# Optimization experiments

Measured on AMD Instinct MI355X. Metric: run time of the kernel, lower is better.

Reference implementation:

```python
import jax, jax.numpy as jnp
import numpy as np

D_IN = 1024
D_H = 1024
B = 8
T = 4096


def setup_inputs() -> dict:
    key = jax.random.key(0)
    ks = jax.random.split(key, 7)
    s_in = 1.0 / np.sqrt(D_IN)
    s_h = 1.0 / np.sqrt(D_H)
    return {
        "x": jax.random.normal(ks[0], (B, T, D_IN), dtype=jnp.float32),
        "h0": jnp.zeros((B, D_H), dtype=jnp.float32),
        "W_a": jax.random.normal(ks[1], (D_IN, D_H), dtype=jnp.float32) * s_in,
        "b_a": jax.random.normal(ks[2], (D_H,), dtype=jnp.float32),
        "W_b": jax.random.normal(ks[3], (D_IN, D_H), dtype=jnp.float32) * s_in,
        "W_y": jax.random.normal(ks[4], (D_H, D_H), dtype=jnp.float32) * s_h,
        "W_skip": jax.random.normal(ks[5], (D_IN, D_H), dtype=jnp.float32) * s_in,
    }


def reference(x, h0, W_a, b_a, W_b, W_y, W_skip):
    # forward_map f: X -> H (monoid element = (decay a, accumulated input b))
    a = jax.nn.sigmoid(jnp.einsum("btd,de->bte", x, W_a) + b_a)  # [B,T,D_H]
    b = jnp.einsum("btd,de->bte", x, W_b)                        # [B,T,D_H]

    # prepend initial carry as monoid element (1, h0), then associative scan
    a_all = jnp.concatenate([jnp.ones_like(h0)[:, None, :], a], axis=1)  # [B,T+1,D_H]
    b_all = jnp.concatenate([h0[:, None, :], b], axis=1)                 # [B,T+1,D_H]

    def monoid_op(l, r):
        a1, b1 = l
        a2, b2 = r
        return (a1 * a2, a2 * b1 + b2)

    _, h_all = jax.lax.associative_scan(monoid_op, (a_all, b_all), axis=1)
    next_h = h_all[:, 1:]  # [B,T,D_H] recurrent states

    # backward_map g: H x X -> Y
    y = jnp.einsum("btd,de->bte", jax.nn.gelu(next_h), W_y) + jnp.einsum("btd,de->bte", x, W_skip)
    return (next_h, y)
```

## Files before the change

### kernel.cpp

```cpp
#include <hip/hip_runtime.h>
#include <stdint.h>

#define D_HID 1024
#define BATCH 8
#define TLEN 4096
#define M_ROWS (BATCH*TLEN)
#define CHUNK 128
#define NCHUNK (TLEN/CHUNK)

typedef __attribute__((ext_vector_type(8))) short s8v;
typedef __attribute__((ext_vector_type(4))) float f4v;

__device__ __forceinline__ ushort f2bf(float x){
  uint32_t u = __builtin_bit_cast(uint32_t, x);
  uint32_t r = u + 0x7fffu + ((u>>16)&1u);
  return (ushort)(r>>16);
}

__device__ __forceinline__ void gload_lds16(const ushort* g, ushort* l){
  __builtin_amdgcn_global_load_lds(
      (const __attribute__((address_space(1))) uint32_t*)g,
      (__attribute__((address_space(3))) uint32_t*)l, 16, 0, 0);
}

__global__ void k_cvt(const float* __restrict__ in, ushort* __restrict__ out, int n4){
  int i = blockIdx.x*blockDim.x + threadIdx.x;
  if (i >= n4) return;
  float4 v = ((const float4*)in)[i];
  ushort4 o;
  o.x = f2bf(v.x); o.y = f2bf(v.y); o.z = f2bf(v.z); o.w = f2bf(v.w);
  ((ushort4*)out)[i] = o;
}

__global__ void k_tr4(const float* __restrict__ s0, const float* __restrict__ s1,
                      const float* __restrict__ s2, const float* __restrict__ s3,
                      ushort* __restrict__ d0, ushort* __restrict__ d1,
                      ushort* __restrict__ d2, ushort* __restrict__ d3){
  const float* src; ushort* dst; int dstride;
  switch (blockIdx.z){
    case 0:  src=s0; dst=d0; dstride=1024; break;
    case 1:  src=s1; dst=d1; dstride=1024; break;
    case 2:  src=s2; dst=d2; dstride=2048; break;
    default: src=s3; dst=d3; dstride=2048; break;
  }
  __shared__ float t[32][33];
  int k0 = blockIdx.x*32, n0 = blockIdx.y*32;
  int tx = threadIdx.x, ty = threadIdx.y;
  #pragma unroll
  for (int i=0;i<4;i++) t[ty+i*8][tx] = src[(size_t)(k0+ty+i*8)*D_HID + n0+tx];
  __syncthreads();
  #pragma unroll
  for (int i=0;i<4;i++) dst[(size_t)(n0+ty+i*8)*dstride + k0+tx] = f2bf(t[tx][ty+i*8]);
}

template<int MODE>
__global__ __launch_bounds__(256) void k_gemm(
    const ushort* __restrict__ A0, const ushort* __restrict__ A1,
    const ushort* __restrict__ Bt, int ldb, int K,
    const float* __restrict__ bias,
    float* __restrict__ out0, float* __restrict__ out1)
{
  __shared__ ushort lA[128*32];
  __shared__ ushort lB[128*32];
  int bn = blockIdx.x, bm = blockIdx.y;
  int tid = threadIdx.x;
  int wid = tid>>6, lane = tid&63;
  int wm = wid>>1, wn = wid&1;
  int lr = lane&15, lk = lane>>4;
  f4v acc[4][4] = {};

  for (int kk=0; kk<K; kk+=32){
    const ushort* Asrc;
    if (MODE==2 && kk>=1024) Asrc = A1 + (size_t)bm*128*1024 + (kk-1024);
    else                     Asrc = A0 + (size_t)bm*128*1024 + kk;
    const ushort* Bsrc = Bt + (size_t)bn*128*ldb + kk;
    __syncthreads();
    #pragma unroll
    for (int i=0;i<2;i++){
      int lin = i*256 + tid;
      int row = lin>>2, kq = lin&3;
      gload_lds16(Asrc + (size_t)row*1024 + kq*8, lA + (size_t)lin*8);
      gload_lds16(Bsrc + (size_t)row*ldb  + kq*8, lB + (size_t)lin*8);
    }
    __syncthreads();
    s8v af[4], bfr[4];
    const s8v* A8 = (const s8v*)lA;
    const s8v* B8 = (const s8v*)lB;
    #pragma unroll
    for (int m=0;m<4;m++) af[m] = A8[(wm*64+m*16+lr)*4 + lk];
    #pragma unroll
    for (int n=0;n<4;n++) bfr[n] = B8[(wn*64+n*16+lr)*4 + lk];
    #pragma unroll
    for (int m=0;m<4;m++)
      #pragma unroll
      for (int n=0;n<4;n++)
        acc[m][n] = __builtin_amdgcn_mfma_f32_16x16x32_bf16(af[m], bfr[n], acc[m][n], 0,0,0);
  }

  int baseRow = bm*128 + wm*64;
  int baseCol = bn*128 + wn*64;
  #pragma unroll
  for (int m=0;m<4;m++){
    #pragma unroll
    for (int n=0;n<4;n++){
      int col = baseCol + n*16 + lr;
      #pragma unroll
      for (int r=0;r<4;r++){
        int row = baseRow + m*16 + lk*4 + r;
        float v = acc[m][n][r];
        if (MODE==1){
          if (col < 1024){
            float s = v + bias[col];
            s = 1.f/(1.f + __expf(-s));
            out0[(size_t)row*1024 + col] = s;
          } else {
            out1[(size_t)row*1024 + (col-1024)] = v;
          }
        } else {
          out0[(size_t)row*1024 + col] = v;
        }
      }
    }
  }
}

__global__ void k_scanA(const float* __restrict__ aw, const float* __restrict__ bw,
                        float* __restrict__ stA, float* __restrict__ stB){
  int d = blockIdx.z*256 + threadIdx.x;
  int c = blockIdx.x, b = blockIdx.y;
  size_t base = ((size_t)(b*TLEN + c*CHUNK))*D_HID + d;
  float Ap = 1.f, Bc = 0.f;
  #pragma unroll 4
  for (int t=0;t<CHUNK;t++){
    float a  = aw[base + (size_t)t*D_HID];
    float bb = bw[base + (size_t)t*D_HID];
    Ap *= a;
    Bc = fmaf(a, Bc, bb);
  }
  size_t si = ((size_t)(b*NCHUNK + c))*D_HID + d;
  stA[si] = Ap; stB[si] = Bc;
}

__global__ void k_scanB(const float* __restrict__ h0, const float* __restrict__ stA,
                        const float* __restrict__ stB, float* __restrict__ hstart){
  int idx = blockIdx.x*256 + threadIdx.x;
  float h = h0[idx];
  int b = idx>>10, d = idx&1023;
  for (int c=0;c<NCHUNK;c++){
    size_t si = ((size_t)(b*NCHUNK+c))*D_HID + d;
    hstart[si] = h;
    h = fmaf(stA[si], h, stB[si]);
  }
}

__global__ void k_scanC(const float* __restrict__ aw, const float* bw,
                        const float* __restrict__ hstart,
                        float* hout, ushort* __restrict__ gws){
  int d = blockIdx.z*256 + threadIdx.x;
  int c = blockIdx.x, b = blockIdx.y;
  size_t base = ((size_t)(b*TLEN + c*CHUNK))*D_HID + d;
  float h = hstart[((size_t)(b*NCHUNK+c))*D_HID + d];
  #pragma unroll 4
  for (int t=0;t<CHUNK;t++){
    float a  = aw[base + (size_t)t*D_HID];
    float bb = bw[base + (size_t)t*D_HID];
    h = fmaf(a, h, bb);
    hout[base + (size_t)t*D_HID] = h;
    float u = 1.5957691216057308f*(h + 0.044715f*h*h*h);
    float g = h * (1.f/(1.f + __expf(-u)));
    gws[base + (size_t)t*D_HID] = f2bf(g);
  }
}

extern "C" void kernel_launch(void* const* d_in, const int* in_sizes, int n_in,
                              void* d_out, int out_size, void* d_ws, size_t ws_size,
                              hipStream_t stream){
  const float* x      = (const float*)d_in[0];
  const float* h0     = (const float*)d_in[1];
  const float* W_a    = (const float*)d_in[2];
  const float* b_a    = (const float*)d_in[3];
  const float* W_b    = (const float*)d_in[4];
  const float* W_y    = (const float*)d_in[5];
  const float* W_skip = (const float*)d_in[6];
  float* out_h = (float*)d_out;
  float* out_y = out_h + (size_t)M_ROWS*D_HID;

  float* aw = out_y;
  float* bw = out_h;

  char* ws = (char*)d_ws;
  ushort* xb    = (ushort*)(ws);
  ushort* gws   = (ushort*)(ws + ((size_t)64<<20));
  ushort* WcatT = (ushort*)(ws + ((size_t)128<<20));
  ushort* W2T   = (ushort*)(ws + ((size_t)132<<20));
  float*  stA   = (float*)(ws + ((size_t)136<<20));
  float*  stB   = (float*)(ws + ((size_t)137<<20));
  float*  hstart= (float*)(ws + ((size_t)138<<20));

  k_cvt<<<dim3(M_ROWS*D_HID/4/256), 256, 0, stream>>>(x, xb, M_ROWS*D_HID/4);
  k_tr4<<<dim3(32,32,4), dim3(32,8), 0, stream>>>(
      W_a, W_b, W_y, W_skip,
      WcatT, WcatT + (size_t)1024*1024, W2T, W2T + 1024);
  k_gemm<1><<<dim3(16,256), 256, 0, stream>>>(xb, nullptr, WcatT, 1024, 1024, b_a, aw, bw);
  k_scanA<<<dim3(NCHUNK,BATCH,4), 256, 0, stream>>>(aw, bw, stA, stB);
  k_scanB<<<dim3(32), 256, 0, stream>>>(h0, stA, stB, hstart);
  k_scanC<<<dim3(NCHUNK,BATCH,4), 256, 0, stream>>>(aw, bw, hstart, out_h, gws);
  k_gemm<2><<<dim3(8,256), 256, 0, stream>>>(gws, xb, W2T, 2048, 2048, nullptr, out_y, nullptr);
}
```

Baseline: 982.5 us.

## Rewrite GEMM with 256x256 tiles, double-buffered LDS and swizzled layout

Replaces the 128x128 single-buffered bf16 MFMA GEMM with a 512-thread, 256x256-tile kernel. K-step 64 tiles are staged into double-buffered dynamic LDS through direct global-to-LDS loads, with an XOR swizzle to avoid bank conflicts. Loads for the next tile are interleaved with MFMA phases, using explicit waitcnt, barriers and setprio. This targets global-memory latency stalls and raises data reuse per block, at the cost of 128KB LDS per block, higher register pressure and fewer blocks in flight.

```diff
diff --git a/kernel.cpp b/kernel.cpp
--- a/kernel.cpp
+++ b/kernel.cpp
@@ -54,53 +54,95 @@
 }
 
 template<int MODE>
-__global__ __launch_bounds__(256) void k_gemm(
+__global__ __launch_bounds__(512, 2) void k_gemm(
     const ushort* __restrict__ A0, const ushort* __restrict__ A1,
     const ushort* __restrict__ Bt, int ldb, int K,
     const float* __restrict__ bias,
     float* __restrict__ out0, float* __restrict__ out1)
 {
-  __shared__ ushort lA[128*32];
-  __shared__ ushort lB[128*32];
+  extern __shared__ ushort lds_u16[];
+  ushort* lA = lds_u16;
+  ushort* lB = lds_u16 + 32768;
   int bn = blockIdx.x, bm = blockIdx.y;
   int tid = threadIdx.x;
   int wid = tid>>6, lane = tid&63;
-  int wm = wid>>1, wn = wid&1;
+  int wm = wid>>2, wn = wid&3;
   int lr = lane&15, lk = lane>>4;
-  f4v acc[4][4] = {};
-
-  for (int kk=0; kk<K; kk+=32){
-    const ushort* Asrc;
-    if (MODE==2 && kk>=1024) Asrc = A1 + (size_t)bm*128*1024 + (kk-1024);
-    else                     Asrc = A0 + (size_t)bm*128*1024 + kk;
-    const ushort* Bsrc = Bt + (size_t)bn*128*ldb + kk;
-    __syncthreads();
-    #pragma unroll
-    for (int i=0;i<2;i++){
-      int lin = i*256 + tid;
-      int row = lin>>2, kq = lin&3;
-      gload_lds16(Asrc + (size_t)row*1024 + kq*8, lA + (size_t)lin*8);
-      gload_lds16(Bsrc + (size_t)row*ldb  + kq*8, lB + (size_t)lin*8);
+  f4v acc[8][4] = {};
+  s8v a[8];
+  const int NT = K>>6;
+
+  auto stage = [&](int T1, int u, int j, int dslot){
+    int kh  = u>>1;
+    int idx = j*512 + tid;
+    int row = idx>>2;
+    int cb  = (idx&3)<<4;
+    int sc  = cb ^ (((row>>1)&3)<<4);
+    int kg  = T1*64 + kh*32 + (sc>>1);
+    const ushort* g;
+    ushort* l;
+    if (u & 1) {
+      const ushort* Ab = A0; int kk = kg;
+      if (MODE==2 && kg >= 1024) { Ab = A1; kk = kg - 1024; }
+      g = Ab + (size_t)(bm*256 + row)*1024 + kk;
+      l = lA + dslot*16384 + kh*8192 + idx*8;
+    } else {
+      g = Bt + (size_t)(bn*256 + row)*ldb + kg;
+      l = lB + dslot*16384 + kh*8192 + idx*8;
     }
-    __syncthreads();
-    s8v af[4], bfr[4];
-    const s8v* A8 = (const s8v*)lA;
-    const s8v* B8 = (const s8v*)lB;
-    #pragma unroll
-    for (int m=0;m<4;m++) af[m] = A8[(wm*64+m*16+lr)*4 + lk];
-    #pragma unroll
-    for (int n=0;n<4;n++) bfr[n] = B8[(wn*64+n*16+lr)*4 + lk];
-    #pragma unroll
-    for (int m=0;m<4;m++)
-      #pragma unroll
-      for (int n=0;n<4;n++)
-        acc[m][n] = __builtin_amdgcn_mfma_f32_16x16x32_bf16(af[m], bfr[n], acc[m][n], 0,0,0);
-  }
-
-  int baseRow = bm*128 + wm*64;
-  int baseCol = bn*128 + wn*64;
-  #pragma unroll
-  for (int m=0;m<4;m++){
+    gload_lds16(g, l);
+  };
+  auto rdA = [&](int m, int ks, int sl)->s8v{
+    int row = wm*128 + m*16 + lr;
+    int sc  = (lk<<4) ^ (((row>>1)&3)<<4);
+    return *(const s8v*)(lA + sl*16384 + ks*8192 + row*32 + (sc>>1));
+  };
+  auto rdB = [&](int n, int ks, int sl)->s8v{
+    int row = wn*64 + n*16 + lr;
+    int sc  = (lk<<4) ^ (((row>>1)&3)<<4);
+    return *(const s8v*)(lB + sl*16384 + ks*8192 + row*32 + (sc>>1));
+  };
+
+#define PHASE(KS, NH, UST, DOA, ISEND) do {                                   \
+    if (DOA) { _Pragma("unroll")                                              \
+      for (int m_=0; m_<8; ++m_) a[m_] = rdA(m_, KS, s); }                    \
+    s8v b0 = rdB((NH)*2,   KS, s);                                            \
+    s8v b1 = rdB((NH)*2+1, KS, s);                                            \
+    if (T+1 < NT) { stage(T+1, UST, 0, d); stage(T+1, UST, 1, d); }           \
+    __builtin_amdgcn_s_barrier();                                             \
+    asm volatile("s_waitcnt lgkmcnt(0)" ::: "memory");                        \
+    __builtin_amdgcn_s_setprio(1);                                            \
+    _Pragma("unroll")                                                         \
+    for (int m_=0; m_<8; ++m_) {                                              \
+      acc[m_][(NH)*2]   = __builtin_amdgcn_mfma_f32_16x16x32_bf16(a[m_], b0, acc[m_][(NH)*2],   0,0,0); \
+      acc[m_][(NH)*2+1] = __builtin_amdgcn_mfma_f32_16x16x32_bf16(a[m_], b1, acc[m_][(NH)*2+1], 0,0,0); \
+    }                                                                         \
+    __builtin_amdgcn_s_setprio(0);                                            \
+    if (ISEND) {                                                              \
+      if (T+1 < NT) asm volatile("s_waitcnt vmcnt(4)" ::: "memory");          \
+      else          asm volatile("s_waitcnt vmcnt(0)" ::: "memory");          \
+    }                                                                         \
+    __builtin_amdgcn_s_barrier();                                             \
+  } while(0)
+
+  #pragma unroll
+  for (int u=0; u<4; ++u){ stage(0,u,0,0); stage(0,u,1,0); }
+  asm volatile("s_waitcnt vmcnt(4)" ::: "memory");
+  __builtin_amdgcn_s_barrier();
+
+  for (int T=0; T<NT; ++T){
+    int s = T&1, d = s^1;
+    PHASE(0,0, 0, true , false);
+    PHASE(0,1, 1, false, true );
+    PHASE(1,0, 2, true , false);
+    PHASE(1,1, 3, false, true );
+  }
+#undef PHASE
+
+  int baseRow = bm*256 + wm*128;
+  int baseCol = bn*256 + wn*64;
+  #pragma unroll
+  for (int m=0;m<8;m++){
     #pragma unroll
     for (int n=0;n<4;n++){
       int col = baseCol + n*16 + lr;
@@ -110,9 +152,9 @@
         float v = acc[m][n][r];
         if (MODE==1){
           if (col < 1024){
-            float s = v + bias[col];
-            s = 1.f/(1.f + __expf(-s));
-            out0[(size_t)row*1024 + col] = s;
+            float sg = v + bias[col];
+            sg = 1.f/(1.f + __expf(-sg));
+            out0[(size_t)row*1024 + col] = sg;
           } else {
             out1[(size_t)row*1024 + (col-1024)] = v;
           }
@@ -197,13 +239,18 @@
   float*  stB   = (float*)(ws + ((size_t)137<<20));
   float*  hstart= (float*)(ws + ((size_t)138<<20));
 
+  (void)hipFuncSetAttribute((const void*)&k_gemm<1>,
+        hipFuncAttributeMaxDynamicSharedMemorySize, 131072);
+  (void)hipFuncSetAttribute((const void*)&k_gemm<2>,
+        hipFuncAttributeMaxDynamicSharedMemorySize, 131072);
+
   k_cvt<<<dim3(M_ROWS*D_HID/4/256), 256, 0, stream>>>(x, xb, M_ROWS*D_HID/4);
   k_tr4<<<dim3(32,32,4), dim3(32,8), 0, stream>>>(
       W_a, W_b, W_y, W_skip,
       WcatT, WcatT + (size_t)1024*1024, W2T, W2T + 1024);
-  k_gemm<1><<<dim3(16,256), 256, 0, stream>>>(xb, nullptr, WcatT, 1024, 1024, b_a, aw, bw);
+  k_gemm<1><<<dim3(8,128), 512, 131072, stream>>>(xb, nullptr, WcatT, 1024, 1024, b_a, aw, bw);
   k_scanA<<<dim3(NCHUNK,BATCH,4), 256, 0, stream>>>(aw, bw, stA, stB);
   k_scanB<<<dim3(32), 256, 0, stream>>>(h0, stA, stB, hstart);
   k_scanC<<<dim3(NCHUNK,BATCH,4), 256, 0, stream>>>(aw, bw, hstart, out_h, gws);
-  k_gemm<2><<<dim3(8,256), 256, 0, stream>>>(gws, xb, W2T, 2048, 2048, nullptr, out_y, nullptr);
-}
+  k_gemm<2><<<dim3(4,128), 512, 131072, stream>>>(gws, xb, W2T, 2048, 2048, nullptr, out_y, nullptr);
+}
```

Result: faster. 869.1 us (-11.5%).
